# Optimization experiments

Hardware: AMD Instinct MI355X
Metric: run time of the kernel (lower is better)

Reference implementation:

```python
import jax, jax.numpy as jnp
import numpy as np
import math

B, IN_CH, OUT_CH, STYLE, KS, DIL, L = 16, 128, 256, 512, 3, 1, 16384


def setup_inputs() -> dict:
    key = jax.random.key(0)
    ks = jax.random.split(key, 6)
    return {
        "x": jax.random.normal(ks[0], (B, IN_CH, L), jnp.float32),
        "style": jax.random.normal(ks[1], (B, STYLE), jnp.float32),
        "conv_weight": jax.random.normal(ks[2], (1, OUT_CH, IN_CH, KS), jnp.float32),
        "mod_weight": jax.random.normal(ks[3], (IN_CH, STYLE), jnp.float32),
        "mod_bias": jnp.ones((IN_CH,), jnp.float32),  # bias_init=1 in EqualLinear
        "out_v": jax.random.normal(ks[4], (IN_CH, OUT_CH // 2, 1), jnp.float32),
        "out_g": jax.random.uniform(ks[5], (IN_CH, 1, 1), jnp.float32, 0.5, 1.5),
        "out_bias": jnp.zeros((IN_CH,), jnp.float32),
    }


def reference(x, style, conv_weight, mod_weight, mod_bias, out_v, out_g, out_bias):
    scale_conv = 1.0 / math.sqrt(IN_CH * KS ** 2)  # fan_in = in_channel * k**2
    scale_mod = 1.0 / math.sqrt(STYLE)             # EqualLinear scale, lr_mul=1

    # modulation: EqualLinear(style_dim -> in_channel)
    s = style @ (mod_weight * scale_mod).T + mod_bias            # [B, I]

    # per-sample modulated + demodulated conv weight
    w = scale_conv * conv_weight * s[:, None, :, None]           # [B, O, I, K]
    demod = jax.lax.rsqrt(jnp.sum(w * w, axis=(2, 3)) + 1e-8)    # [B, O]
    w = w * demod[:, :, None, None]

    # grouped (groups=batch) dilated conv1d == per-sample conv via unfold + einsum
    pad = (KS - 1) // 2 * DIL
    xp = jnp.pad(x, ((0, 0), (0, 0), (pad, pad)))
    patches = jnp.stack([xp[:, :, k * DIL:k * DIL + L] for k in range(KS)], axis=2)  # [B, I, K, L]
    out = jnp.einsum('boik,bikl->bol', w, patches)               # [B, O, L]

    # gated tanh-sigmoid
    xa, xb = jnp.split(out, 2, axis=1)
    g = jnp.tanh(xa) * jax.nn.sigmoid(xb)                        # [B, O//2, L]

    # weight-normed 1x1 conv (dim=0: norm over in_ch and k per out channel)
    vnorm = jnp.sqrt(jnp.sum(out_v * out_v, axis=(1, 2), keepdims=True))
    w1 = (out_g * out_v / vnorm)[:, :, 0]                        # [R, O//2]
    y = jnp.einsum('oc,bcl->bol', w1, g) + out_bias[None, :, None]

    return (y + x) * math.sqrt(0.5)
```

## Files before the change

### kernel.cpp

```cpp
#include <hip/hip_runtime.h>
#include <hip/hip_bf16.h>
#include <math.h>

typedef float f32x4 __attribute__((ext_vector_type(4)));
typedef short bh8  __attribute__((ext_vector_type(8)));
typedef unsigned int u32x4 __attribute__((ext_vector_type(4)));

#define B_   16
#define IC   128
#define OC   256
#define RC   128
#define STY  512
#define KS_  3
#define LL   16384
#define LT   128

#define WS_S_OFF   0
#define WS_W_OFF   8192
#define WS_W1_OFF  (8192 + 3145728)

#define XS_OFF 0
#define GS_OFF 33280
#define SMEM_BYTES 66048

__device__ __forceinline__ unsigned short f2b(float f) {
    union { float f; unsigned int u; } z; z.f = f;
    unsigned int u = z.u;
    return (unsigned short)((u + 0x7fffu + ((u >> 16) & 1u)) >> 16);
}

__device__ __forceinline__ float b2f(unsigned int u16) {
    union { unsigned int u; float f; } z; z.u = u16 << 16;
    return z.f;
}

__device__ __forceinline__ unsigned int pack2bf(float a, float b) {
    __hip_bfloat162 p = __float22bfloat162_rn(make_float2(a, b));
    return *(unsigned int*)&p;
}

__global__ void k_style(const float* __restrict__ style, const float* __restrict__ mw,
                        const float* __restrict__ mb, float* __restrict__ s_out) {
    const int b = blockIdx.x, i = threadIdx.x;
    const float4* st = (const float4*)(style + b * STY);
    const float4* w  = (const float4*)(mw + (size_t)i * STY);
    float acc = 0.f;
#pragma unroll 4
    for (int j = 0; j < STY / 4; ++j) {
        float4 a = st[j], c = w[j];
        acc += a.x * c.x + a.y * c.y + a.z * c.z + a.w * c.w;
    }
    s_out[b * IC + i] = acc * 0.044194173824159216f + mb[i];
}

__global__ void k_modw(const float* __restrict__ cw, const float* __restrict__ s,
                       unsigned short* __restrict__ wbf) {
    const int o = blockIdx.x, b = blockIdx.y, i = threadIdx.x;
    const float sv = s[b * IC + i] * 0.029462782549439476f;
    const float w0 = cw[(o * IC + i) * KS_ + 0] * sv;
    const float w1 = cw[(o * IC + i) * KS_ + 1] * sv;
    const float w2 = cw[(o * IC + i) * KS_ + 2] * sv;
    float ss = w0 * w0 + w1 * w1 + w2 * w2;
    for (int off = 32; off; off >>= 1) ss += __shfl_down(ss, off, 64);
    __shared__ float red[2];
    if ((i & 63) == 0) red[i >> 6] = ss;
    __syncthreads();
    const float d = rsqrtf(red[0] + red[1] + 1e-8f);
    unsigned short* dst = wbf + ((size_t)b * OC + o) * 384 + i;
    dst[0]   = f2b(w0 * d);
    dst[128] = f2b(w1 * d);
    dst[256] = f2b(w2 * d);
}

__global__ void k_w1(const float* __restrict__ v, const float* __restrict__ g,
                     unsigned short* __restrict__ w1bf) {
    const int o = blockIdx.x, c = threadIdx.x;
    const float vv = v[o * RC + c];
    float ss = vv * vv;
    for (int off = 32; off; off >>= 1) ss += __shfl_down(ss, off, 64);
    __shared__ float red[2];
    if ((c & 63) == 0) red[c >> 6] = ss;
    __syncthreads();
    w1bf[o * RC + c] = f2b(g[o] * vv * rsqrtf(red[0] + red[1]) * 0.70710678118654752f);
}

__global__ __launch_bounds__(512, 4) void k_main(
    const float* __restrict__ x, const unsigned short* __restrict__ wbf,
    const unsigned short* __restrict__ w1bf, const float* __restrict__ obias,
    float* __restrict__ out) {
    __shared__ alignas(16) char smem[SMEM_BYTES];

    const int t = threadIdx.x;
    const int lane = t & 63, wv = t >> 6;
    const int lm = lane & 15, kg = lane >> 4;
    const int c0 = wv * 16 + kg * 4;

    const int lid = blockIdx.x;
    const int swz = (lid & 7) * 256 + (lid >> 3);
    const int b  = swz >> 7;
    const int l0 = (swz & 127) * LT;

    const float* xb = x + (size_t)b * IC * LL + l0;

    {
        const int chb = wv * 16;
#pragma unroll
        for (int p = 0; p < 2; ++p) {
            const int pos = lane + p * 64;
            const int row = pos + 1;
#pragma unroll
            for (int h = 0; h < 2; ++h) {
                float xv[8];
#pragma unroll
                for (int c = 0; c < 8; ++c)
                    xv[c] = xb[(size_t)(chb + h * 8 + c) * LL + pos];
                u32x4 wvec;
                wvec.x = pack2bf(xv[0], xv[1]);
                wvec.y = pack2bf(xv[2], xv[3]);
                wvec.z = pack2bf(xv[4], xv[5]);
                wvec.w = pack2bf(xv[6], xv[7]);
                *(u32x4*)(smem + XS_OFF + row * 256 +
                          (((chb + h * 8) * 2) ^ ((row & 15) << 4))) = wvec;
            }
        }
    }
    if (t < 128) {
        const float* hx = x + ((size_t)b * IC + t) * LL;
        float lf = (l0 > 0) ? hx[l0 - 1] : 0.f;
        float rt = (l0 + LT < LL) ? hx[l0 + LT] : 0.f;
        *(unsigned short*)(smem + XS_OFF + 0 * 256 + ((t * 2) ^ ((0 & 15) << 4)))     = f2b(lf);
        *(unsigned short*)(smem + XS_OFF + 129 * 256 + ((t * 2) ^ ((129 & 15) << 4))) = f2b(rt);
    }
    __syncthreads();

    f32x4 acc[2][8];
#pragma unroll
    for (int m = 0; m < 2; ++m)
#pragma unroll
        for (int nt = 0; nt < 8; ++nt) acc[m][nt] = (f32x4){0.f, 0.f, 0.f, 0.f};

    const unsigned short* wa = wbf + ((size_t)b * OC + wv * 16 + lm) * 384 + kg * 8;
    const unsigned short* wb2 = wa + 128 * 384;

    bh8 ca0 = *(const bh8*)(wa + 0);
    bh8 ca1 = *(const bh8*)(wb2 + 0);
#pragma unroll
    for (int kc = 0; kc < 12; ++kc) {
        bh8 na0 = ca0, na1 = ca1;
        if (kc < 11) {
            const int nkoff = ((kc + 1) >> 2) * 128 + ((kc + 1) & 3) * 32;
            na0 = *(const bh8*)(wa + nkoff);
            na1 = *(const bh8*)(wb2 + nkoff);
        }
        const int tap = kc >> 2;
        const int icb = (kc & 3) * 32;
#pragma unroll
        for (int nt = 0; nt < 8; ++nt) {
            const int lr = nt * 16 + lm + tap;
            const bh8 bf = *(const bh8*)(smem + XS_OFF + lr * 256 +
                                         (((icb + kg * 8) * 2) ^ ((lr & 15) << 4)));
            acc[0][nt] = __builtin_amdgcn_mfma_f32_16x16x32_bf16(ca0, bf, acc[0][nt], 0, 0, 0);
            acc[1][nt] = __builtin_amdgcn_mfma_f32_16x16x32_bf16(ca1, bf, acc[1][nt], 0, 0, 0);
        }
        ca0 = na0; ca1 = na1;
    }

#pragma unroll
    for (int nt = 0; nt < 8; ++nt) {
        float g4[4];
#pragma unroll
        for (int j = 0; j < 4; ++j) {
            const float xa = acc[0][nt][j], xg = acc[1][nt][j];
            const float th = 1.f - 2.f * __builtin_amdgcn_rcpf(__expf(2.f * xa) + 1.f);
            const float sg = __builtin_amdgcn_rcpf(1.f + __expf(-xg));
            g4[j] = th * sg;
        }
        const int n = nt * 16 + lm;
        *(unsigned long long*)(smem + GS_OFF + n * 256 + ((c0 * 2) ^ ((n & 15) << 4))) =
            (unsigned long long)pack2bf(g4[0], g4[1]) |
            ((unsigned long long)pack2bf(g4[2], g4[3]) << 32);
    }

    const int myc = wv * 16 + lm;
    const unsigned short* w1p = w1bf + (size_t)myc * RC + kg * 8;
    bh8 w1f[4];
#pragma unroll
    for (int kc = 0; kc < 4; ++kc) w1f[kc] = *(const bh8*)(w1p + kc * 32);
    __syncthreads();

    const float bias = obias[myc];
    const float* xrow = x + ((size_t)b * IC + myc) * LL + l0 + kg * 4;
    float* orow = out + ((size_t)b * IC + myc) * LL + l0 + kg * 4;
#pragma unroll
    for (int m = 0; m < 8; ++m) {
        f32x4 acc2 = (f32x4){0.f, 0.f, 0.f, 0.f};
#pragma unroll
        for (int kc = 0; kc < 4; ++kc) {
            const int n = m * 16 + lm;
            const bh8 ga = *(const bh8*)(smem + GS_OFF + n * 256 +
                                         (((kc * 32 + kg * 8) * 2) ^ ((n & 15) << 4)));
            acc2 = __builtin_amdgcn_mfma_f32_16x16x32_bf16(ga, w1f[kc], acc2, 0, 0, 0);
        }
        const float4 xv = *(const float4*)(xrow + m * 16);
        float4 ov;
        ov.x = acc2[0] + (xv.x + bias) * 0.70710678118654752f;
        ov.y = acc2[1] + (xv.y + bias) * 0.70710678118654752f;
        ov.z = acc2[2] + (xv.z + bias) * 0.70710678118654752f;
        ov.w = acc2[3] + (xv.w + bias) * 0.70710678118654752f;
        *(float4*)(orow + m * 16) = ov;
    }
}

extern "C" void kernel_launch(void* const* d_in, const int* in_sizes, int n_in,
                              void* d_out, int out_size, void* d_ws, size_t ws_size,
                              hipStream_t stream) {
    (void)in_sizes; (void)n_in; (void)out_size; (void)ws_size;
    const float* x        = (const float*)d_in[0];
    const float* style    = (const float*)d_in[1];
    const float* conv_w   = (const float*)d_in[2];
    const float* mod_w    = (const float*)d_in[3];
    const float* mod_b    = (const float*)d_in[4];
    const float* out_v    = (const float*)d_in[5];
    const float* out_g    = (const float*)d_in[6];
    const float* out_bias = (const float*)d_in[7];
    float* out = (float*)d_out;

    float* s_buf = (float*)((char*)d_ws + WS_S_OFF);
    unsigned short* wbf  = (unsigned short*)((char*)d_ws + WS_W_OFF);
    unsigned short* w1bf = (unsigned short*)((char*)d_ws + WS_W1_OFF);

    k_style<<<dim3(B_), 128, 0, stream>>>(style, mod_w, mod_b, s_buf);
    k_modw<<<dim3(OC, B_), 128, 0, stream>>>(conv_w, s_buf, wbf);
    k_w1<<<dim3(RC), 128, 0, stream>>>(out_v, out_g, w1bf);
    k_main<<<dim3(B_ * LL / LT), 512, 0, stream>>>(x, wbf, w1bf, out_bias, out);
}
```

Before: 129.5 us.

## Use 32x32 MFMA for modulated conv and reuse LDS x for residual

Switches the per-sample modulated conv GEMM from 16x16x32 to 32x32x16 bf16 MFMA tiles, remapping waves to 32 output channels by 64 positions, which improves operand reuse per LDS fetch. The residual term is now taken from the bf16 x tile already staged in shared memory and preloaded as the accumulator of the 1x1 conv, removing a second fp32 global read of x. This trades residual precision (bf16 instead of fp32) for less HBM traffic.

Result: slower. 168.9 us (+30.4%).

```diff
diff --git a/kernel.cpp b/kernel.cpp
--- a/kernel.cpp
+++ b/kernel.cpp
@@ -2,7 +2,8 @@
 #include <hip/hip_bf16.h>
 #include <math.h>
 
-typedef float f32x4 __attribute__((ext_vector_type(4)));
+typedef float f32x4  __attribute__((ext_vector_type(4)));
+typedef float f32x16 __attribute__((ext_vector_type(16)));
 typedef short bh8  __attribute__((ext_vector_type(8)));
 typedef unsigned int u32x4 __attribute__((ext_vector_type(4)));
 
@@ -93,7 +94,9 @@
     const int t = threadIdx.x;
     const int lane = t & 63, wv = t >> 6;
     const int lm = lane & 15, kg = lane >> 4;
-    const int c0 = wv * 16 + kg * 4;
+    const int l31 = lane & 31, hk = lane >> 5;
+    const int w2 = wv >> 1;
+    const int nb = (wv & 1) * 64;
 
     const int lid = blockIdx.x;
     const int swz = (lid & 7) * 256 + (lid >> 3);
@@ -133,67 +136,85 @@
     }
     __syncthreads();
 
-    f32x4 acc[2][8];
+    f32x16 acc[2][2];
 #pragma unroll
     for (int m = 0; m < 2; ++m)
 #pragma unroll
-        for (int nt = 0; nt < 8; ++nt) acc[m][nt] = (f32x4){0.f, 0.f, 0.f, 0.f};
-
-    const unsigned short* wa = wbf + ((size_t)b * OC + wv * 16 + lm) * 384 + kg * 8;
-    const unsigned short* wb2 = wa + 128 * 384;
-
-    bh8 ca0 = *(const bh8*)(wa + 0);
-    bh8 ca1 = *(const bh8*)(wb2 + 0);
-#pragma unroll
-    for (int kc = 0; kc < 12; ++kc) {
+        for (int n = 0; n < 2; ++n)
+#pragma unroll
+            for (int e = 0; e < 16; ++e) acc[m][n][e] = 0.f;
+
+    const unsigned short* wa0 = wbf + ((size_t)b * OC + 32 * w2 + l31) * 384 + hk * 8;
+
+    bh8 ca0 = *(const bh8*)(wa0 + 0);
+    bh8 ca1 = *(const bh8*)(wa0 + 128 * 384);
+#pragma unroll
+    for (int kc = 0; kc < 24; ++kc) {
         bh8 na0 = ca0, na1 = ca1;
-        if (kc < 11) {
-            const int nkoff = ((kc + 1) >> 2) * 128 + ((kc + 1) & 3) * 32;
-            na0 = *(const bh8*)(wa + nkoff);
-            na1 = *(const bh8*)(wb2 + nkoff);
-        }
-        const int tap = kc >> 2;
-        const int icb = (kc & 3) * 32;
-#pragma unroll
-        for (int nt = 0; nt < 8; ++nt) {
-            const int lr = nt * 16 + lm + tap;
-            const bh8 bf = *(const bh8*)(smem + XS_OFF + lr * 256 +
-                                         (((icb + kg * 8) * 2) ^ ((lr & 15) << 4)));
-            acc[0][nt] = __builtin_amdgcn_mfma_f32_16x16x32_bf16(ca0, bf, acc[0][nt], 0, 0, 0);
-            acc[1][nt] = __builtin_amdgcn_mfma_f32_16x16x32_bf16(ca1, bf, acc[1][nt], 0, 0, 0);
+        if (kc < 23) {
+            const int nkoff = ((kc + 1) >> 3) * 128 + ((kc + 1) & 7) * 16;
+            na0 = *(const bh8*)(wa0 + nkoff);
+            na1 = *(const bh8*)(wa0 + 128 * 384 + nkoff);
+        }
+        const int tap = kc >> 3;
+        const int icb = (kc & 7) * 16;
+#pragma unroll
+        for (int nch = 0; nch < 2; ++nch) {
+            const int row = nb + 32 * nch + l31 + tap;
+            const bh8 bf = *(const bh8*)(smem + XS_OFF + row * 256 +
+                                         (((icb + hk * 8) * 2) ^ ((row & 15) << 4)));
+            acc[0][nch] = __builtin_amdgcn_mfma_f32_32x32x16_bf16(ca0, bf, acc[0][nch], 0, 0, 0);
+            acc[1][nch] = __builtin_amdgcn_mfma_f32_32x32x16_bf16(ca1, bf, acc[1][nch], 0, 0, 0);
         }
         ca0 = na0; ca1 = na1;
     }
 
 #pragma unroll
-    for (int nt = 0; nt < 8; ++nt) {
-        float g4[4];
+    for (int nch = 0; nch < 2; ++nch) {
+        const int row = nb + 32 * nch + l31;
+#pragma unroll
+        for (int q = 0; q < 4; ++q) {
+            float g4[4];
+#pragma unroll
+            for (int e = 0; e < 4; ++e) {
+                const int r = q * 4 + e;
+                const float xa = acc[0][nch][r], xg = acc[1][nch][r];
+                const float th = 1.f - 2.f * __builtin_amdgcn_rcpf(__expf(2.f * xa) + 1.f);
+                const float sg = __builtin_amdgcn_rcpf(1.f + __expf(-xg));
+                g4[e] = th * sg;
+            }
+            const int cb = 32 * w2 + 8 * q + 4 * hk;
+            *(unsigned long long*)(smem + GS_OFF + row * 256 +
+                                   ((cb * 2) ^ ((row & 15) << 4))) =
+                (unsigned long long)pack2bf(g4[0], g4[1]) |
+                ((unsigned long long)pack2bf(g4[2], g4[3]) << 32);
+        }
+    }
+
+    const int myc = wv * 16 + lm;
+    const float bias = obias[myc];
+    f32x4 cin[8];
+#pragma unroll
+    for (int m = 0; m < 8; ++m) {
 #pragma unroll
         for (int j = 0; j < 4; ++j) {
-            const float xa = acc[0][nt][j], xg = acc[1][nt][j];
-            const float th = 1.f - 2.f * __builtin_amdgcn_rcpf(__expf(2.f * xa) + 1.f);
-            const float sg = __builtin_amdgcn_rcpf(1.f + __expf(-xg));
-            g4[j] = th * sg;
-        }
-        const int n = nt * 16 + lm;
-        *(unsigned long long*)(smem + GS_OFF + n * 256 + ((c0 * 2) ^ ((n & 15) << 4))) =
-            (unsigned long long)pack2bf(g4[0], g4[1]) |
-            ((unsigned long long)pack2bf(g4[2], g4[3]) << 32);
-    }
-
-    const int myc = wv * 16 + lm;
+            const int row = m * 16 + kg * 4 + j + 1;
+            const unsigned int xu = *(const unsigned short*)(
+                smem + XS_OFF + row * 256 + ((myc * 2) ^ ((row & 15) << 4)));
+            cin[m][j] = (b2f(xu) + bias) * 0.70710678118654752f;
+        }
+    }
+
     const unsigned short* w1p = w1bf + (size_t)myc * RC + kg * 8;
     bh8 w1f[4];
 #pragma unroll
     for (int kc = 0; kc < 4; ++kc) w1f[kc] = *(const bh8*)(w1p + kc * 32);
     __syncthreads();
 
-    const float bias = obias[myc];
-    const float* xrow = x + ((size_t)b * IC + myc) * LL + l0 + kg * 4;
     float* orow = out + ((size_t)b * IC + myc) * LL + l0 + kg * 4;
 #pragma unroll
     for (int m = 0; m < 8; ++m) {
-        f32x4 acc2 = (f32x4){0.f, 0.f, 0.f, 0.f};
+        f32x4 acc2 = cin[m];
 #pragma unroll
         for (int kc = 0; kc < 4; ++kc) {
             const int n = m * 16 + lm;
@@ -201,12 +222,7 @@
                                          (((kc * 32 + kg * 8) * 2) ^ ((n & 15) << 4)));
             acc2 = __builtin_amdgcn_mfma_f32_16x16x32_bf16(ga, w1f[kc], acc2, 0, 0, 0);
         }
-        const float4 xv = *(const float4*)(xrow + m * 16);
-        float4 ov;
-        ov.x = acc2[0] + (xv.x + bias) * 0.70710678118654752f;
-        ov.y = acc2[1] + (xv.y + bias) * 0.70710678118654752f;
-        ov.z = acc2[2] + (xv.z + bias) * 0.70710678118654752f;
-        ov.w = acc2[3] + (xv.w + bias) * 0.70710678118654752f;
+        float4 ov; ov.x = acc2[0]; ov.y = acc2[1]; ov.z = acc2[2]; ov.w = acc2[3];
         *(float4*)(orow + m * 16) = ov;
     }
 }
```
